# Performance work log

Hardware: AMD Instinct MI355X
Metric: run time of the kernel (lower is better)

Reference implementation:

```python
import jax, jax.numpy as jnp
import numpy as np

N, K, D_IN, H = 8192, 8, 512, 512
SCALE = 0.02  # weight init scale


def setup_inputs() -> dict:
    key = jax.random.key(0)
    ks = jax.random.split(key, 12)
    inp = {
        "x": jax.random.normal(ks[0], (N, D_IN), jnp.float32),
        "child_h": jax.random.normal(ks[1], (N, K, H), jnp.float32),
        "child_c": jax.random.normal(ks[2], (N, K, H), jnp.float32),
    }
    names = ["i", "f", "o", "u"]
    for idx, g in enumerate(names):
        inp["W" + g] = jax.random.normal(ks[3 + idx], (D_IN, H), jnp.float32) * SCALE
        inp["bW" + g] = jnp.zeros((H,), jnp.float32)
        inp["U" + g] = jax.random.normal(ks[7 + idx], (H, H), jnp.float32) * SCALE
        inp["bU" + g] = jnp.zeros((H,), jnp.float32)
    return inp


def reference(x, child_h, child_c,
              Wi, bWi, Ui, bUi,
              Wf, bWf, Uf, bUf,
              Wo, bWo, Uo, bUo,
              Wu, bWu, Uu, bUu):
    # Child-Sum Tree-LSTM, batched over N nodes each with K children.
    h_sum = child_h.sum(axis=1)                                   # [N, H]
    i = jax.nn.sigmoid(x @ Wi + bWi + h_sum @ Ui + bUi)           # [N, H]
    o = jax.nn.sigmoid(x @ Wo + bWo + h_sum @ Uo + bUo)           # [N, H]
    u = jnp.tanh(x @ Wu + bWu + h_sum @ Uu + bUu)                 # [N, H]
    # Per-child forget gates: f_k = sigmoid(W_f x + U_f h_k)
    f = jax.nn.sigmoid((x @ Wf + bWf)[:, None, :]
                       + jnp.einsum('nkh,hg->nkg', child_h, Uf) + bUf)  # [N, K, H]
    c = i * u + (f * child_c).sum(axis=1)                         # [N, H]
    h = o * jnp.tanh(c)                                           # [N, H]
    return jnp.stack([h, c], axis=0)                              # [2, N, H]
```

## Files before the change

kernel.cpp:

```cpp
#include <hip/hip_runtime.h>
#include <hip/hip_bf16.h>


#define NN 8192
#define KCH 8
#define HH 512

typedef __attribute__((ext_vector_type(4))) float f32x4;
typedef __attribute__((ext_vector_type(8))) short short8;

__device__ inline unsigned short f2bf(float f) {
    union { float f; unsigned u; } v; v.f = f;
    unsigned r = v.u + 0x7FFFu + ((v.u >> 16) & 1u);
    return (unsigned short)(r >> 16);
}
__device__ inline float bf2f(unsigned short b) {
    union { unsigned u; float f; } v; v.u = ((unsigned)b) << 16;
    return v.f;
}
__device__ inline float sigm(float x) { return 1.f / (1.f + __expf(-x)); }
__device__ inline float tanh_pf(float x) { return 2.f / (1.f + __expf(-2.f * x)) - 1.f; }


__global__ void k_cvt(const float* __restrict__ in, unsigned short* __restrict__ outp) {
    int i = blockIdx.x * blockDim.x + threadIdx.x;
    float4 a = ((const float4*)in)[2 * i];
    float4 b = ((const float4*)in)[2 * i + 1];
    uint4 o;
    o.x = (unsigned)f2bf(a.x) | ((unsigned)f2bf(a.y) << 16);
    o.y = (unsigned)f2bf(a.z) | ((unsigned)f2bf(a.w) << 16);
    o.z = (unsigned)f2bf(b.x) | ((unsigned)f2bf(b.y) << 16);
    o.w = (unsigned)f2bf(b.z) | ((unsigned)f2bf(b.w) << 16);
    ((uint4*)outp)[i] = o;
}

__global__ void k_hsum(const float* __restrict__ ch, unsigned short* __restrict__ hs) {
    int i = blockIdx.x * blockDim.x + threadIdx.x;
    int n = i >> 7, h4 = i & 127;
    const float4* base = (const float4*)(ch + (size_t)n * KCH * HH) + h4;
    float4 s = base[0];
#pragma unroll
    for (int k = 1; k < KCH; ++k) {
        float4 v = base[(size_t)k * 128];
        s.x += v.x; s.y += v.y; s.z += v.z; s.w += v.w;
    }
    unsigned long long pk = (unsigned long long)f2bf(s.x)
        | ((unsigned long long)f2bf(s.y) << 16)
        | ((unsigned long long)f2bf(s.z) << 32)
        | ((unsigned long long)f2bf(s.w) << 48);
    *(unsigned long long*)&hs[(size_t)i * 4] = pk;
}

struct P8 { const float* p[8]; };
__global__ void k_transpose_w(P8 wsrc, unsigned short* __restrict__ out) {
    __shared__ float tile[32][33];
    const float* W = wsrc.p[blockIdx.z];
    unsigned short* O = out + (size_t)blockIdx.z * 262144;
    int k0 = blockIdx.x * 32, c0 = blockIdx.y * 32;
    for (int r = threadIdx.y; r < 32; r += 8)
        tile[r][threadIdx.x] = W[(size_t)(k0 + r) * 512 + c0 + threadIdx.x];
    __syncthreads();
    for (int r = threadIdx.y; r < 32; r += 8)
        O[(size_t)(c0 + r) * 512 + k0 + threadIdx.x] = f2bf(tile[threadIdx.x][r]);
}


__device__ inline void stage_a(unsigned short (*a_lds)[40], const unsigned short* A,
                               int r0, int k0, int t) {
#pragma unroll
    for (int p = 0; p < 2; ++p) {
        int li = p * 256 + t;
        int row = li >> 2, c8 = (li & 3) * 8;
        *(uint4*)&a_lds[row][c8] = *(const uint4*)&A[(size_t)(r0 + row) * 512 + k0 + c8];
    }
}
__device__ inline void stage_b64(unsigned short (*b_lds)[40], const unsigned short* BT,
                                 int c0, int k0, int t) {
    int col = t >> 2, c8 = (t & 3) * 8;
    *(uint4*)&b_lds[col][c8] = *(const uint4*)&BT[(size_t)(c0 + col) * 512 + k0 + c8];
}

__device__ inline void gate_mfma(f32x4 (&acc)[4][2], const short8 (&af)[4],
                                 const unsigned short (*bl)[40], int bcol, int koff) {
    short8 b0 = *(const short8*)&bl[bcol][koff];
    short8 b1 = *(const short8*)&bl[bcol + 16][koff];
#pragma unroll
    for (int m = 0; m < 4; ++m) {
        acc[m][0] = __builtin_amdgcn_mfma_f32_16x16x32_bf16(af[m], b0, acc[m][0], 0, 0, 0);
        acc[m][1] = __builtin_amdgcn_mfma_f32_16x16x32_bf16(af[m], b1, acc[m][1], 0, 0, 0);
    }
}

__global__ __launch_bounds__(256) void k_gates(
    const unsigned short* __restrict__ xb,
    const unsigned short* __restrict__ hsb,
    const unsigned short* __restrict__ wT,
    const float* __restrict__ bWi, const float* __restrict__ bUi,
    const float* __restrict__ bWf,
    const float* __restrict__ bWo, const float* __restrict__ bUo,
    const float* __restrict__ bWu, const float* __restrict__ bUu,
    unsigned short* __restrict__ Pq,
    unsigned short* __restrict__ Oq,
    unsigned short* __restrict__ Fq)
{
    __shared__ unsigned short a_lds[128][40];
    __shared__ unsigned short b_lds[4][64][40];
    const int t = threadIdx.x, lane = t & 63, wid = t >> 6;
    const int wr = wid >> 1, wc = wid & 1;
    const int r0 = blockIdx.y * 128, c0 = blockIdx.x * 64;

    f32x4 acc_i[4][2] = {}; f32x4 acc_f[4][2] = {};
    f32x4 acc_o[4][2] = {}; f32x4 acc_u[4][2] = {};

    const int koff = (lane >> 4) * 8;
    const int arow = wr * 64 + (lane & 15);
    const int bcol = wc * 32 + (lane & 15);

    for (int kq = 0; kq < 512; kq += 32) {
        __syncthreads();
        stage_a(a_lds, xb, r0, kq, t);
        stage_b64(b_lds[0], wT + (size_t)0 * 262144, c0, kq, t);
        stage_b64(b_lds[1], wT + (size_t)2 * 262144, c0, kq, t);
        stage_b64(b_lds[2], wT + (size_t)3 * 262144, c0, kq, t);
        stage_b64(b_lds[3], wT + (size_t)5 * 262144, c0, kq, t);
        __syncthreads();
        short8 af[4];
#pragma unroll
        for (int m = 0; m < 4; ++m) af[m] = *(const short8*)&a_lds[arow + m * 16][koff];
        gate_mfma(acc_i, af, b_lds[0], bcol, koff);
        gate_mfma(acc_f, af, b_lds[1], bcol, koff);
        gate_mfma(acc_o, af, b_lds[2], bcol, koff);
        gate_mfma(acc_u, af, b_lds[3], bcol, koff);
    }
    for (int kq = 0; kq < 512; kq += 32) {
        __syncthreads();
        stage_a(a_lds, hsb, r0, kq, t);
        stage_b64(b_lds[0], wT + (size_t)1 * 262144, c0, kq, t);
        stage_b64(b_lds[1], wT + (size_t)4 * 262144, c0, kq, t);
        stage_b64(b_lds[2], wT + (size_t)6 * 262144, c0, kq, t);
        __syncthreads();
        short8 af[4];
#pragma unroll
        for (int m = 0; m < 4; ++m) af[m] = *(const short8*)&a_lds[arow + m * 16][koff];
        gate_mfma(acc_i, af, b_lds[0], bcol, koff);
        gate_mfma(acc_o, af, b_lds[1], bcol, koff);
        gate_mfma(acc_u, af, b_lds[2], bcol, koff);
    }
#pragma unroll
    for (int m = 0; m < 4; ++m) {
#pragma unroll
        for (int n = 0; n < 2; ++n) {
            int col = c0 + wc * 32 + n * 16 + (lane & 15);
            float bi = bWi[col] + bUi[col];
            float bf = bWf[col];
            float bo = bWo[col] + bUo[col];
            float bu = bWu[col] + bUu[col];
#pragma unroll
            for (int r = 0; r < 4; ++r) {
                int row = r0 + wr * 64 + m * 16 + (lane >> 4) * 4 + r;
                size_t idx = (size_t)row * 512 + col;
                float vi = sigm(acc_i[m][n][r] + bi);
                float vu = tanh_pf(acc_u[m][n][r] + bu);
                Pq[idx] = f2bf(vi * vu);
                Oq[idx] = f2bf(sigm(acc_o[m][n][r] + bo));
                Fq[idx] = f2bf(acc_f[m][n][r] + bf);
            }
        }
    }
}

__global__ __launch_bounds__(256) void k_fc(
    const float* __restrict__ ch,
    const float* __restrict__ cc,
    const unsigned short* __restrict__ ufT,
    const float* __restrict__ bUf,
    const unsigned short* __restrict__ Pq,
    const unsigned short* __restrict__ Oq,
    const unsigned short* __restrict__ Fq,
    float* __restrict__ out)
{
    __shared__ union LdsU {
        struct { unsigned short a[128][40]; unsigned short b[128][40]; } s;
        float f[128][128];
    } u;
    const int t = threadIdx.x, lane = t & 63, wid = t >> 6;
    const int wr = wid >> 1, wc = wid & 1;
    const int r0 = blockIdx.y * 128, c0 = blockIdx.x * 128;

    f32x4 acc[4][4] = {};
    const int koff = (lane >> 4) * 8;
    const int arow = wr * 64 + (lane & 15);
    const int bcol = wc * 64 + (lane & 15);

    for (int kq = 0; kq < 512; kq += 32) {
        __syncthreads();
#pragma unroll
        for (int p = 0; p < 4; ++p) {
            int li = p * 256 + t;
            int row = li >> 3, c4 = (li & 7) * 4;
            float4 v = *(const float4*)&ch[(size_t)(r0 + row) * 512 + kq + c4];
            unsigned long long pk = (unsigned long long)f2bf(v.x)
                | ((unsigned long long)f2bf(v.y) << 16)
                | ((unsigned long long)f2bf(v.z) << 32)
                | ((unsigned long long)f2bf(v.w) << 48);
            *(unsigned long long*)&u.s.a[row][c4] = pk;
        }
#pragma unroll
        for (int p = 0; p < 2; ++p) {
            int li = p * 256 + t;
            int col = li >> 2, c8 = (li & 3) * 8;
            *(uint4*)&u.s.b[col][c8] = *(const uint4*)&ufT[(size_t)(c0 + col) * 512 + kq + c8];
        }
        __syncthreads();
        short8 af[4], bfr[4];
#pragma unroll
        for (int m = 0; m < 4; ++m) af[m] = *(const short8*)&u.s.a[arow + m * 16][koff];
#pragma unroll
        for (int n = 0; n < 4; ++n) bfr[n] = *(const short8*)&u.s.b[bcol + n * 16][koff];
#pragma unroll
        for (int m = 0; m < 4; ++m)
#pragma unroll
            for (int n = 0; n < 4; ++n)
                acc[m][n] = __builtin_amdgcn_mfma_f32_16x16x32_bf16(af[m], bfr[n], acc[m][n], 0, 0, 0);
    }
    __syncthreads();
#pragma unroll
    for (int m = 0; m < 4; ++m)
#pragma unroll
        for (int n = 0; n < 4; ++n)
#pragma unroll
            for (int r = 0; r < 4; ++r)
                u.f[wr * 64 + m * 16 + (lane >> 4) * 4 + r][wc * 64 + n * 16 + (lane & 15)] = acc[m][n][r];
    __syncthreads();
    const int j = t & 127, q = t >> 7;
    for (int ni = q; ni < 16; ni += 2) {
        int node = (r0 >> 3) + ni;
        int col = c0 + j;
        size_t nidx = (size_t)node * 512 + col;
        float xf = bf2f(Fq[nidx]) + bUf[col];
        float fc = 0.f;
#pragma unroll
        for (int k = 0; k < 8; ++k) {
            float pre = u.f[ni * 8 + k][j] + xf;
            float fg = sigm(pre);
            fc += fg * cc[(size_t)(r0 + ni * 8 + k) * 512 + col];
        }
        float cval = bf2f(Pq[nidx]) + fc;
        float h = bf2f(Oq[nidx]) * tanh_pf(cval);
        out[nidx] = h;
        out[(size_t)NN * HH + nidx] = cval;
    }
}

extern "C" void kernel_launch(void* const* d_in, const int* in_sizes, int n_in,
                              void* d_out, int out_size, void* d_ws, size_t ws_size,
                              hipStream_t stream) {
    const float* x   = (const float*)d_in[0];
    const float* ch  = (const float*)d_in[1];
    const float* cc  = (const float*)d_in[2];
    const float* Wi  = (const float*)d_in[3];  const float* bWi = (const float*)d_in[4];
    const float* Ui  = (const float*)d_in[5];  const float* bUi = (const float*)d_in[6];
    const float* Wf  = (const float*)d_in[7];  const float* bWf = (const float*)d_in[8];
    const float* Uf  = (const float*)d_in[9];  const float* bUf = (const float*)d_in[10];
    const float* Wo  = (const float*)d_in[11]; const float* bWo = (const float*)d_in[12];
    const float* Uo  = (const float*)d_in[13]; const float* bUo = (const float*)d_in[14];
    const float* Wu  = (const float*)d_in[15]; const float* bWu = (const float*)d_in[16];
    const float* Uu  = (const float*)d_in[17]; const float* bUu = (const float*)d_in[18];
    float* out = (float*)d_out;

    unsigned short* xb  = (unsigned short*)d_ws;
    unsigned short* hsb = xb  + (size_t)NN * HH;
    unsigned short* wT  = hsb + (size_t)NN * HH;
    unsigned short* Pq  = wT  + (size_t)8 * 262144;
    unsigned short* Oq  = Pq  + (size_t)NN * HH;
    unsigned short* Fq  = Oq  + (size_t)NN * HH;

    k_cvt<<<(NN * HH / 8) / 256, 256, 0, stream>>>(x, xb);
    k_hsum<<<(NN * 128) / 256, 256, 0, stream>>>(ch, hsb);
    P8 wp;
    wp.p[0] = Wi; wp.p[1] = Ui; wp.p[2] = Wf; wp.p[3] = Wo;
    wp.p[4] = Uo; wp.p[5] = Wu; wp.p[6] = Uu; wp.p[7] = Uf;
    k_transpose_w<<<dim3(16, 16, 8), dim3(32, 8), 0, stream>>>(wp, wT);
    k_gates<<<dim3(8, 64), 256, 0, stream>>>(xb, hsb, wT,
                                             bWi, bUi, bWf, bWo, bUo, bWu, bUu,
                                             Pq, Oq, Fq);
    k_fc<<<dim3(4, 512), 256, 0, stream>>>(ch, cc, wT + (size_t)7 * 262144, bUf,
                                           Pq, Oq, Fq, out);
}
```

Baseline: 255.9 us.

## Use direct global-to-LDS loads and restructure forget-cell kernel tiling

Both GEMM kernels now stage tiles into shared memory with global_load_lds 16-byte loads instead of register round trips, which also drops the row padding. The forget/cell kernel is retiled so each 512-thread block covers 64 rows and all 512 columns. Each child_h row is therefore read and converted to bf16 only once, not once per column block. The forget-gate epilogue now works straight from MFMA accumulators with a lane shuffle, removing the fp32 LDS round trip. The risks are LDS bank conflicts from the unpadded layout and a full weight-tile reload per block.

```diff
diff --git a/kernel.cpp b/kernel.cpp
--- a/kernel.cpp
+++ b/kernel.cpp
@@ -20,6 +20,13 @@
 }
 __device__ inline float sigm(float x) { return 1.f / (1.f + __expf(-x)); }
 __device__ inline float tanh_pf(float x) { return 2.f / (1.f + __expf(-2.f * x)) - 1.f; }
+
+__device__ __forceinline__ void gl16(const unsigned short* gsrc, unsigned short* ldst) {
+    __builtin_amdgcn_global_load_lds(
+        (const __attribute__((address_space(1))) unsigned int*)gsrc,
+        (__attribute__((address_space(3))) unsigned int*)ldst,
+        16, 0, 0);
+}
 
 
 __global__ void k_cvt(const float* __restrict__ in, unsigned short* __restrict__ outp) {
@@ -62,33 +69,6 @@
     __syncthreads();
     for (int r = threadIdx.y; r < 32; r += 8)
         O[(size_t)(c0 + r) * 512 + k0 + threadIdx.x] = f2bf(tile[threadIdx.x][r]);
-}
-
-
-__device__ inline void stage_a(unsigned short (*a_lds)[40], const unsigned short* A,
-                               int r0, int k0, int t) {
-#pragma unroll
-    for (int p = 0; p < 2; ++p) {
-        int li = p * 256 + t;
-        int row = li >> 2, c8 = (li & 3) * 8;
-        *(uint4*)&a_lds[row][c8] = *(const uint4*)&A[(size_t)(r0 + row) * 512 + k0 + c8];
-    }
-}
-__device__ inline void stage_b64(unsigned short (*b_lds)[40], const unsigned short* BT,
-                                 int c0, int k0, int t) {
-    int col = t >> 2, c8 = (t & 3) * 8;
-    *(uint4*)&b_lds[col][c8] = *(const uint4*)&BT[(size_t)(c0 + col) * 512 + k0 + c8];
-}
-
-__device__ inline void gate_mfma(f32x4 (&acc)[4][2], const short8 (&af)[4],
-                                 const unsigned short (*bl)[40], int bcol, int koff) {
-    short8 b0 = *(const short8*)&bl[bcol][koff];
-    short8 b1 = *(const short8*)&bl[bcol + 16][koff];
-#pragma unroll
-    for (int m = 0; m < 4; ++m) {
-        acc[m][0] = __builtin_amdgcn_mfma_f32_16x16x32_bf16(af[m], b0, acc[m][0], 0, 0, 0);
-        acc[m][1] = __builtin_amdgcn_mfma_f32_16x16x32_bf16(af[m], b1, acc[m][1], 0, 0, 0);
-    }
 }
 
 __global__ __launch_bounds__(256) void k_gates(
@@ -103,8 +83,8 @@
     unsigned short* __restrict__ Oq,
     unsigned short* __restrict__ Fq)
 {
-    __shared__ unsigned short a_lds[128][40];
-    __shared__ unsigned short b_lds[4][64][40];
+    __shared__ unsigned short a_lds[128][32];
+    __shared__ unsigned short b_lds[4][64][32];
     const int t = threadIdx.x, lane = t & 63, wid = t >> 6;
     const int wr = wid >> 1, wc = wid & 1;
     const int r0 = blockIdx.y * 128, c0 = blockIdx.x * 64;
@@ -115,36 +95,45 @@
     const int koff = (lane >> 4) * 8;
     const int arow = wr * 64 + (lane & 15);
     const int bcol = wc * 32 + (lane & 15);
-
-    for (int kq = 0; kq < 512; kq += 32) {
-        __syncthreads();
-        stage_a(a_lds, xb, r0, kq, t);
-        stage_b64(b_lds[0], wT + (size_t)0 * 262144, c0, kq, t);
-        stage_b64(b_lds[1], wT + (size_t)2 * 262144, c0, kq, t);
-        stage_b64(b_lds[2], wT + (size_t)3 * 262144, c0, kq, t);
-        stage_b64(b_lds[3], wT + (size_t)5 * 262144, c0, kq, t);
-        __syncthreads();
-        short8 af[4];
-#pragma unroll
-        for (int m = 0; m < 4; ++m) af[m] = *(const short8*)&a_lds[arow + m * 16][koff];
-        gate_mfma(acc_i, af, b_lds[0], bcol, koff);
-        gate_mfma(acc_f, af, b_lds[1], bcol, koff);
-        gate_mfma(acc_o, af, b_lds[2], bcol, koff);
-        gate_mfma(acc_u, af, b_lds[3], bcol, koff);
-    }
-    for (int kq = 0; kq < 512; kq += 32) {
-        __syncthreads();
-        stage_a(a_lds, hsb, r0, kq, t);
-        stage_b64(b_lds[0], wT + (size_t)1 * 262144, c0, kq, t);
-        stage_b64(b_lds[1], wT + (size_t)4 * 262144, c0, kq, t);
-        stage_b64(b_lds[2], wT + (size_t)6 * 262144, c0, kq, t);
-        __syncthreads();
-        short8 af[4];
-#pragma unroll
-        for (int m = 0; m < 4; ++m) af[m] = *(const short8*)&a_lds[arow + m * 16][koff];
-        gate_mfma(acc_i, af, b_lds[0], bcol, koff);
-        gate_mfma(acc_o, af, b_lds[1], bcol, koff);
-        gate_mfma(acc_u, af, b_lds[2], bcol, koff);
+    const int rsub = lane >> 2, c8 = (lane & 3) * 8;
+
+#pragma unroll 1
+    for (int phase = 0; phase < 2; ++phase) {
+        const unsigned short* Asrc = phase ? hsb : xb;
+        const unsigned short* Bbase = wT + (size_t)(phase ? 4 : 0) * 262144;
+        const int nchunk = phase ? 20 : 24;
+#pragma unroll 1
+        for (int kq = 0; kq < 512; kq += 32) {
+            __syncthreads();
+            for (int c = wid; c < nchunk; c += 4) {
+                if (c < 8) {
+                    gl16(&Asrc[(size_t)(r0 + c * 16 + rsub) * 512 + kq + c8],
+                         &a_lds[c * 16][0]);
+                } else {
+                    int d = c - 8, p = d >> 2, cb = d & 3;
+                    gl16(&Bbase[(size_t)p * 262144 + (size_t)(c0 + cb * 16 + rsub) * 512 + kq + c8],
+                         &b_lds[p][cb * 16][0]);
+                }
+            }
+            __syncthreads();
+            short8 af[4];
+#pragma unroll
+            for (int m = 0; m < 4; ++m) af[m] = *(const short8*)&a_lds[arow + m * 16][koff];
+#pragma unroll
+            for (int p = 0; p < 4; ++p) {
+                if (phase && p == 3) break;
+                short8 b0 = *(const short8*)&b_lds[p][bcol][koff];
+                short8 b1 = *(const short8*)&b_lds[p][bcol + 16][koff];
+                f32x4 (*acc)[2] = (phase == 0)
+                    ? (p == 0 ? acc_i : p == 1 ? acc_f : p == 2 ? acc_o : acc_u)
+                    : (p == 0 ? acc_i : p == 1 ? acc_o : acc_u);
+#pragma unroll
+                for (int m = 0; m < 4; ++m) {
+                    acc[m][0] = __builtin_amdgcn_mfma_f32_16x16x32_bf16(af[m], b0, acc[m][0], 0, 0, 0);
+                    acc[m][1] = __builtin_amdgcn_mfma_f32_16x16x32_bf16(af[m], b1, acc[m][1], 0, 0, 0);
+                }
+            }
+        }
     }
 #pragma unroll
     for (int m = 0; m < 4; ++m) {
@@ -169,7 +158,7 @@
     }
 }
 
-__global__ __launch_bounds__(256) void k_fc(
+__global__ __launch_bounds__(512, 2) void k_fc(
     const float* __restrict__ ch,
     const float* __restrict__ cc,
     const unsigned short* __restrict__ ufT,
@@ -179,76 +168,70 @@
     const unsigned short* __restrict__ Fq,
     float* __restrict__ out)
 {
-    __shared__ union LdsU {
-        struct { unsigned short a[128][40]; unsigned short b[128][40]; } s;
-        float f[128][128];
-    } u;
+    __shared__ unsigned short a_lds[64][32];
+    __shared__ unsigned short b_lds[512][32];
     const int t = threadIdx.x, lane = t & 63, wid = t >> 6;
-    const int wr = wid >> 1, wc = wid & 1;
-    const int r0 = blockIdx.y * 128, c0 = blockIdx.x * 128;
+    const int wc = wid;
+    const int r0c = blockIdx.x * 64;
 
     f32x4 acc[4][4] = {};
     const int koff = (lane >> 4) * 8;
-    const int arow = wr * 64 + (lane & 15);
-    const int bcol = wc * 64 + (lane & 15);
-
+    const int rsub = lane >> 2, cb8 = (lane & 3) * 8;
+    const int sarow = t >> 3, sac4 = (t & 7) * 4;
+
+#pragma unroll 1
     for (int kq = 0; kq < 512; kq += 32) {
         __syncthreads();
-#pragma unroll
-        for (int p = 0; p < 4; ++p) {
-            int li = p * 256 + t;
-            int row = li >> 3, c4 = (li & 7) * 4;
-            float4 v = *(const float4*)&ch[(size_t)(r0 + row) * 512 + kq + c4];
+        {
+            float4 v = *(const float4*)&ch[(size_t)(r0c + sarow) * 512 + kq + sac4];
             unsigned long long pk = (unsigned long long)f2bf(v.x)
                 | ((unsigned long long)f2bf(v.y) << 16)
                 | ((unsigned long long)f2bf(v.z) << 32)
                 | ((unsigned long long)f2bf(v.w) << 48);
-            *(unsigned long long*)&u.s.a[row][c4] = pk;
-        }
-#pragma unroll
-        for (int p = 0; p < 2; ++p) {
-            int li = p * 256 + t;
-            int col = li >> 2, c8 = (li & 3) * 8;
-            *(uint4*)&u.s.b[col][c8] = *(const uint4*)&ufT[(size_t)(c0 + col) * 512 + kq + c8];
-        }
+            *(unsigned long long*)&a_lds[sarow][sac4] = pk;
+        }
+        for (int c = wid; c < 32; c += 8)
+            gl16(&ufT[(size_t)(c * 16 + rsub) * 512 + kq + cb8], &b_lds[c * 16][0]);
         __syncthreads();
         short8 af[4], bfr[4];
 #pragma unroll
-        for (int m = 0; m < 4; ++m) af[m] = *(const short8*)&u.s.a[arow + m * 16][koff];
-#pragma unroll
-        for (int n = 0; n < 4; ++n) bfr[n] = *(const short8*)&u.s.b[bcol + n * 16][koff];
+        for (int m = 0; m < 4; ++m) af[m] = *(const short8*)&a_lds[m * 16 + (lane & 15)][koff];
+#pragma unroll
+        for (int n = 0; n < 4; ++n) bfr[n] = *(const short8*)&b_lds[wc * 64 + n * 16 + (lane & 15)][koff];
 #pragma unroll
         for (int m = 0; m < 4; ++m)
 #pragma unroll
             for (int n = 0; n < 4; ++n)
                 acc[m][n] = __builtin_amdgcn_mfma_f32_16x16x32_bf16(af[m], bfr[n], acc[m][n], 0, 0, 0);
     }
-    __syncthreads();
-#pragma unroll
-    for (int m = 0; m < 4; ++m)
-#pragma unroll
-        for (int n = 0; n < 4; ++n)
-#pragma unroll
-            for (int r = 0; r < 4; ++r)
-                u.f[wr * 64 + m * 16 + (lane >> 4) * 4 + r][wc * 64 + n * 16 + (lane & 15)] = acc[m][n][r];
-    __syncthreads();
-    const int j = t & 127, q = t >> 7;
-    for (int ni = q; ni < 16; ni += 2) {
-        int node = (r0 >> 3) + ni;
-        int col = c0 + j;
-        size_t nidx = (size_t)node * 512 + col;
-        float xf = bf2f(Fq[nidx]) + bUf[col];
-        float fc = 0.f;
-#pragma unroll
-        for (int k = 0; k < 8; ++k) {
-            float pre = u.f[ni * 8 + k][j] + xf;
-            float fg = sigm(pre);
-            fc += fg * cc[(size_t)(r0 + ni * 8 + k) * 512 + col];
-        }
-        float cval = bf2f(Pq[nidx]) + fc;
-        float h = bf2f(Oq[nidx]) * tanh_pf(cval);
-        out[nidx] = h;
-        out[(size_t)NN * HH + nidx] = cval;
+
+    const int g = lane >> 4;
+    float bUfv[4];
+#pragma unroll
+    for (int n = 0; n < 4; ++n) bUfv[n] = bUf[wc * 64 + n * 16 + (lane & 15)];
+
+#pragma unroll
+    for (int m = 0; m < 4; ++m) {
+        int node = (r0c >> 3) + 2 * m + (g >> 1);
+#pragma unroll
+        for (int n = 0; n < 4; ++n) {
+            int col = wc * 64 + n * 16 + (lane & 15);
+            size_t nidx = (size_t)node * 512 + col;
+            float xf = bf2f(Fq[nidx]) + bUfv[n];
+            float fcs = 0.f;
+#pragma unroll
+            for (int r = 0; r < 4; ++r) {
+                int R = r0c + m * 16 + g * 4 + r;
+                float pre = acc[m][n][r] + xf;
+                fcs += sigm(pre) * cc[(size_t)R * 512 + col];
+            }
+            fcs += __shfl_xor(fcs, 16);
+            if ((g & 1) == 0) {
+                float cv = bf2f(Pq[nidx]) + fcs;
+                out[nidx] = bf2f(Oq[nidx]) * tanh_pf(cv);
+                out[(size_t)NN * HH + nidx] = cv;
+            }
+        }
     }
 }
 
@@ -278,12 +261,12 @@
     k_cvt<<<(NN * HH / 8) / 256, 256, 0, stream>>>(x, xb);
     k_hsum<<<(NN * 128) / 256, 256, 0, stream>>>(ch, hsb);
     P8 wp;
-    wp.p[0] = Wi; wp.p[1] = Ui; wp.p[2] = Wf; wp.p[3] = Wo;
-    wp.p[4] = Uo; wp.p[5] = Wu; wp.p[6] = Uu; wp.p[7] = Uf;
+    wp.p[0] = Wi; wp.p[1] = Wf; wp.p[2] = Wo; wp.p[3] = Wu;
+    wp.p[4] = Ui; wp.p[5] = Uo; wp.p[6] = Uu; wp.p[7] = Uf;
     k_transpose_w<<<dim3(16, 16, 8), dim3(32, 8), 0, stream>>>(wp, wT);
     k_gates<<<dim3(8, 64), 256, 0, stream>>>(xb, hsb, wT,
                                              bWi, bUi, bWf, bWo, bUo, bWu, bUu,
                                              Pq, Oq, Fq);
-    k_fc<<<dim3(4, 512), 256, 0, stream>>>(ch, cc, wT + (size_t)7 * 262144, bUf,
-                                           Pq, Oq, Fq, out);
-}
+    k_fc<<<dim3(1024), 512, 0, stream>>>(ch, cc, wT + (size_t)7 * 262144, bUf,
+                                         Pq, Oq, Fq, out);
+}
```

New measurement: 557.0 us. +117.7%, slower.
